# Kernel tuning notes

Hardware: AMD Instinct MI355X
Metric: run time of the kernel (lower is better)

Reference implementation:

```python
import jax, jax.numpy as jnp
import numpy as np

D_MODEL = 768
NUM_HEADS = 12
D_K = D_MODEL // NUM_HEADS


def setup_inputs() -> dict:
    key = jax.random.key(0)
    ks = jax.random.split(key, 9)
    B, S = 2, 4096
    x = jax.random.normal(ks[0], (B, S, D_MODEL), dtype=jnp.float32)
    s = 1.0 / np.sqrt(D_MODEL)
    Wq = jax.random.normal(ks[1], (D_MODEL, D_MODEL), dtype=jnp.float32) * s
    Wk = jax.random.normal(ks[2], (D_MODEL, D_MODEL), dtype=jnp.float32) * s
    Wv = jax.random.normal(ks[3], (D_MODEL, D_MODEL), dtype=jnp.float32) * s
    Wo = jax.random.normal(ks[4], (D_MODEL, D_MODEL), dtype=jnp.float32) * s
    bq = jnp.zeros((D_MODEL,), dtype=jnp.float32)
    bk = jnp.zeros((D_MODEL,), dtype=jnp.float32)
    bv = jnp.zeros((D_MODEL,), dtype=jnp.float32)
    bo = jnp.zeros((D_MODEL,), dtype=jnp.float32)
    return {"x": x, "Wq": Wq, "bq": bq, "Wk": Wk, "bk": bk,
            "Wv": Wv, "bv": bv, "Wo": Wo, "bo": bo}


def _split_heads(t):
    B, S, _ = t.shape
    return t.reshape(B, S, NUM_HEADS, D_K).transpose(0, 2, 1, 3)  # [B,H,S,d_k]


def reference(x, Wq, bq, Wk, bk, Wv, bv, Wo, bo):
    Q = _split_heads(x @ Wq.T + bq)
    K = _split_heads(x @ Wk.T + bk)
    V = _split_heads(x @ Wv.T + bv)
    scale = 1.0 / jnp.sqrt(jnp.float32(D_K))
    scores = jnp.einsum('bhqd,bhkd->bhqk', Q, K) * scale  # [B,H,S,S]
    attn = jax.nn.softmax(scores, axis=-1)
    out = jnp.einsum('bhqk,bhkd->bhqd', attn, V)          # [B,H,S,d_k]
    B, _, S, _ = out.shape
    out = out.transpose(0, 2, 1, 3).reshape(B, S, D_MODEL)
    return out @ Wo.T + bo
```

## Files before the change

kernel.cpp:

```cpp
#include <hip/hip_runtime.h>
#include <hip/hip_bf16.h>
#include <stdint.h>

typedef __hip_bfloat16 bf16;
typedef __attribute__((ext_vector_type(8))) short short8;
typedef __attribute__((ext_vector_type(4))) float f32x4;
typedef __attribute__((ext_vector_type(16))) float f32x16;

#define MFMA16(a, b, c) __builtin_amdgcn_mfma_f32_16x16x32_bf16((a), (b), (c), 0, 0, 0)
#define MFMA32(a, b, c) __builtin_amdgcn_mfma_f32_32x32x16_bf16((a), (b), (c), 0, 0, 0)

__device__ __forceinline__ unsigned short f2bf(float f) {
  bf16 h = __float2bfloat16(f);
  unsigned short u;
  __builtin_memcpy(&u, &h, 2);
  return u;
}

__device__ __forceinline__ uint32_t cvtpk(float lo, float hi) {
  uint32_t r;
  asm("v_cvt_pk_bf16_f32 %0, %1, %2" : "=v"(r) : "v"(lo), "v"(hi));
  return r;
}

__device__ __forceinline__ void pl32swap(uint32_t& a, uint32_t& b) {
  asm volatile("v_permlane32_swap_b32 %0, %1" : "+v"(a), "+v"(b));
}

__device__ __forceinline__ void gload_lds16(const void* g, void* l) {
  __builtin_amdgcn_global_load_lds(
      (const __attribute__((address_space(1))) uint32_t*)g,
      (__attribute__((address_space(3))) uint32_t*)l, 16, 0, 0);
}

__device__ __forceinline__ int swz_chunk(int row, int c) { return c ^ (row & 7); }

__global__ __launch_bounds__(256) void cvt_all(
    const float* __restrict__ x,
    const float* __restrict__ w0, const float* __restrict__ w1,
    const float* __restrict__ w2, const float* __restrict__ w3,
    bf16* __restrict__ xo,
    bf16* __restrict__ o0, bf16* __restrict__ o1,
    bf16* __restrict__ o2, bf16* __restrict__ o3) {
  int idx = blockIdx.x * 256 + threadIdx.x;
  const float* src;
  bf16* dst;
  int i;
  if (idx < 1572864) {
    src = x; dst = xo; i = idx;
  } else {
    int r = idx - 1572864;
    int w = r / 147456;
    i = r - w * 147456;
    src = (w == 0) ? w0 : (w == 1) ? w1 : (w == 2) ? w2 : w3;
    dst = (w == 0) ? o0 : (w == 1) ? o1 : (w == 2) ? o2 : o3;
  }
  float4 v = ((const float4*)src)[i];
  ushort4 u;
  u.x = f2bf(v.x); u.y = f2bf(v.y); u.z = f2bf(v.z); u.w = f2bf(v.w);
  ((ushort4*)dst)[i] = u;
}

__global__ __launch_bounds__(256, 4) void gemm_qkv(
    const bf16* __restrict__ A,
    const bf16* __restrict__ Wqb, const bf16* __restrict__ Wkb,
    const bf16* __restrict__ Wvb,
    const float* __restrict__ bq, const float* __restrict__ bk,
    const float* __restrict__ bv,
    bf16* __restrict__ Qh, bf16* __restrict__ Kh, bf16* __restrict__ Vh,
    float sq) {
  __shared__ bf16 As[128 * 64];
  __shared__ bf16 Bs[128 * 64];
  const int tid = threadIdx.x;
  const int lane = tid & 63, wid = tid >> 6;
  const int wr = wid >> 1, wc = wid & 1;
  const int l15 = lane & 15, lhi = lane >> 4;
  const int tm = blockIdx.x * 128;
  const int by = blockIdx.y;
  const int seg = by / 6;
  const int tn = (by - seg * 6) * 128;

  const bf16* B = (seg == 0) ? Wqb : (seg == 1) ? Wkb : Wvb;
  const float* bias = (seg == 0) ? bq : (seg == 1) ? bk : bv;
  bf16* dst = (seg == 0) ? Qh : (seg == 1) ? Kh : Vh;
  const float scale = (seg == 0) ? sq : 1.0f;
  const int K = 768;

  f32x4 zero = {0.f, 0.f, 0.f, 0.f};
  f32x4 acc[4][4];
  for (int i = 0; i < 4; ++i)
    for (int j = 0; j < 4; ++j) acc[i][j] = zero;

  for (int k0 = 0; k0 < K; k0 += 64) {
    __syncthreads();
    for (int it = 0; it < 4; ++it) {
      int o = (tid + it * 256) << 4;
      int row = o >> 7, c = (o >> 4) & 7;
      int sw = swz_chunk(row, c) << 4;
      gload_lds16((const char*)A + (((size_t)(tm + row) * K + k0) << 1) + sw, (char*)As + o);
      gload_lds16((const char*)B + (((size_t)(tn + row) * K + k0) << 1) + sw, (char*)Bs + o);
    }
    __syncthreads();
    for (int ks = 0; ks < 2; ++ks) {
      short8 af[4], bfr[4];
      for (int mi = 0; mi < 4; ++mi) {
        int row = wr * 64 + mi * 16 + l15;
        af[mi] = *(const short8*)((const char*)As + row * 128 +
                                  (swz_chunk(row, ks * 4 + lhi) << 4));
      }
      for (int ni = 0; ni < 4; ++ni) {
        int row = wc * 64 + ni * 16 + l15;
        bfr[ni] = *(const short8*)((const char*)Bs + row * 128 +
                                   (swz_chunk(row, ks * 4 + lhi) << 4));
      }
      for (int mi = 0; mi < 4; ++mi)
        for (int ni = 0; ni < 4; ++ni)
          acc[mi][ni] = MFMA16(af[mi], bfr[ni], acc[mi][ni]);
    }
  }

  for (int mi = 0; mi < 4; ++mi)
    for (int ni = 0; ni < 4; ++ni)
      for (int j = 0; j < 4; ++j) {
        int m = tm + wr * 64 + mi * 16 + lhi * 4 + j;
        int n = tn + wc * 64 + ni * 16 + l15;
        float v = (acc[mi][ni][j] + bias[n]) * scale;
        int b = m >> 12, s = m & 4095, h = n >> 6, d = n & 63;
        dst[(((size_t)(b * 12 + h) * 4096 + s) << 6) + d] = __float2bfloat16(v);
      }
}

__global__ __launch_bounds__(256, 4) void gemm_wo(
    const bf16* __restrict__ A, const bf16* __restrict__ B,
    const float* __restrict__ bias, float* __restrict__ C) {
  __shared__ bf16 As[128 * 64];
  __shared__ bf16 Bs[64 * 64];
  const int tid = threadIdx.x;
  const int lane = tid & 63, wid = tid >> 6;
  const int l15 = lane & 15, lhi = lane >> 4;
  const int tm = blockIdx.x * 128, tn = blockIdx.y * 64;
  const int K = 768;

  f32x4 zero = {0.f, 0.f, 0.f, 0.f};
  f32x4 acc[2][4];
  for (int i = 0; i < 2; ++i)
    for (int j = 0; j < 4; ++j) acc[i][j] = zero;

  for (int k0 = 0; k0 < K; k0 += 64) {
    __syncthreads();
    for (int it = 0; it < 4; ++it) {
      int o = (tid + it * 256) << 4;
      int row = o >> 7, c = (o >> 4) & 7;
      int sw = swz_chunk(row, c) << 4;
      gload_lds16((const char*)A + (((size_t)(tm + row) * K + k0) << 1) + sw, (char*)As + o);
    }
    for (int it = 0; it < 2; ++it) {
      int o = (tid + it * 256) << 4;
      int row = o >> 7, c = (o >> 4) & 7;
      int sw = swz_chunk(row, c) << 4;
      gload_lds16((const char*)B + (((size_t)(tn + row) * K + k0) << 1) + sw, (char*)Bs + o);
    }
    __syncthreads();
    for (int ks = 0; ks < 2; ++ks) {
      short8 af[2], bfr[4];
      for (int mi = 0; mi < 2; ++mi) {
        int row = wid * 32 + mi * 16 + l15;
        af[mi] = *(const short8*)((const char*)As + row * 128 +
                                  (swz_chunk(row, ks * 4 + lhi) << 4));
      }
      for (int ni = 0; ni < 4; ++ni) {
        int row = ni * 16 + l15;
        bfr[ni] = *(const short8*)((const char*)Bs + row * 128 +
                                   (swz_chunk(row, ks * 4 + lhi) << 4));
      }
      for (int mi = 0; mi < 2; ++mi)
        for (int ni = 0; ni < 4; ++ni)
          acc[mi][ni] = MFMA16(af[mi], bfr[ni], acc[mi][ni]);
    }
  }

  for (int mi = 0; mi < 2; ++mi)
    for (int ni = 0; ni < 4; ++ni)
      for (int j = 0; j < 4; ++j) {
        int m = tm + wid * 32 + mi * 16 + lhi * 4 + j;
        int n = tn + ni * 16 + l15;
        C[(size_t)m * 768 + n] = acc[mi][ni][j] + bias[n];
      }
}

__global__ __launch_bounds__(256) void transpose_v(const bf16* __restrict__ Vh,
                                                   bf16* __restrict__ VTh) {
  __shared__ bf16 T[64 * 64];
  const int tid = threadIdx.x;
  const int bh = blockIdx.x >> 6;
  const int t = blockIdx.x & 63;
  const char* src = (const char*)(Vh + ((size_t)bh * 4096 + t * 64) * 64);
  char* dst = (char*)(VTh + ((size_t)bh * 64) * 4096 + t * 64);

  const int rp = tid & 31, cc = tid >> 5;
  uint4 va = *(const uint4*)(src + (2 * rp) * 128 + cc * 16);
  uint4 vb = *(const uint4*)(src + (2 * rp + 1) * 128 + cc * 16);
  unsigned short a16[8], b16[8];
  __builtin_memcpy(a16, &va, 16);
  __builtin_memcpy(b16, &vb, 16);
#pragma unroll
  for (int jj = 0; jj < 8; ++jj) {
    uint32_t w = (uint32_t)a16[jj] | ((uint32_t)b16[jj] << 16);
    *(uint32_t*)((char*)T + (cc * 8 + jj) * 128 + (((rp >> 2) ^ jj) << 4) +
                 ((rp & 3) << 2)) = w;
  }
  __syncthreads();
  for (int it = 0; it < 2; ++it) {
    int idx = tid + it * 256;
    int d = idx >> 3, c = idx & 7;
    uint4 vv = *(const uint4*)((const char*)T + d * 128 + (swz_chunk(d, c) << 4));
    *(uint4*)(dst + (size_t)d * 8192 + c * 16) = vv;
  }
}

__global__ __launch_bounds__(256, 3) void attn_kernel(
    const bf16* __restrict__ Qh, const bf16* __restrict__ Kh,
    const bf16* __restrict__ VTh, bf16* __restrict__ AO) {
  __shared__ float4 smem4[34816 / 16];
  char* smraw = (char*)smem4;
#define KT(b) (smraw + (b) * 8192)
#define VT(b) (smraw + 16384 + (b) * 8192)
  float* OX = (float*)smraw;

  const int tid = threadIdx.x;
  const int lane = tid & 63, wid = tid >> 6;
  const int l31 = lane & 31, h = lane >> 5;
  const int qsub = wid & 1, kvh = wid >> 1;

  const int i = blockIdx.x;
  const int xcd = i & 7, slot = i >> 3;
  const int bh = xcd * 3 + (slot >> 5);
  const int qt = slot & 31;

  const size_t hb = (size_t)bh * 4096 * 64;
  const bf16* Qb = Qh + hb;
  const bf16* Kb = Kh + hb;
  const char* Vg0 = (const char*)(VTh + hb);
  const int qb = qt * 128 + qsub * 64;

  short8 qf[2][4];
#pragma unroll
  for (int j = 0; j < 2; ++j)
#pragma unroll
    for (int ki = 0; ki < 4; ++ki)
      qf[j][ki] = *(const short8*)((const char*)Qb + (size_t)(qb + 32 * j + l31) * 128 +
                                   ki * 32 + h * 16);

  f32x16 z16;
  for (int i2 = 0; i2 < 16; ++i2) z16[i2] = 0.f;
  f32x16 o00 = z16, o01 = z16, o10 = z16, o11 = z16;
  float psum0 = 0.f, psum1 = 0.f;

  const int krow = kvh * 32 + l31;

  for (int it = 0; it < 2; ++it) {
    int o = (tid + it * 256) << 4;
    int row = o >> 7, c = (o >> 4) & 7;
    int sw = swz_chunk(row, c) << 4;
    gload_lds16((const char*)Kb + row * 128 + sw, KT(0) + o);
    gload_lds16(Vg0 + row * 8192 + sw, VT(0) + o);
  }
  __syncthreads();

  int cur = 0;
  for (int kt = 0; kt < 64; ++kt) {
    if (kt < 63) {
      const char* Kg = (const char*)(Kb + (size_t)(kt + 1) * 4096);
      const char* Vg = Vg0 + (size_t)(kt + 1) * 128;
      char* Kd = KT(cur ^ 1);
      char* Vd = VT(cur ^ 1);
      for (int it = 0; it < 2; ++it) {
        int o = (tid + it * 256) << 4;
        int row = o >> 7, c = (o >> 4) & 7;
        int sw = swz_chunk(row, c) << 4;
        gload_lds16(Kg + row * 128 + sw, Kd + o);
        gload_lds16(Vg + row * 8192 + sw, Vd + o);
      }
    }

    const char* Kl = KT(cur);
    const char* Vl = VT(cur);

    f32x16 s0, s1;
    __builtin_amdgcn_s_setprio(1);
    {
      short8 kf = *(const short8*)(Kl + krow * 128 + (swz_chunk(krow, h) << 4));
      s0 = MFMA32(kf, qf[0][0], z16);
      s1 = MFMA32(kf, qf[1][0], z16);
    }
#pragma unroll
    for (int ki = 1; ki < 4; ++ki) {
      short8 kf = *(const short8*)(Kl + krow * 128 + (swz_chunk(krow, 2 * ki + h) << 4));
      s0 = MFMA32(kf, qf[0][ki], s0);
      s1 = MFMA32(kf, qf[1][ki], s1);
    }
    __builtin_amdgcn_s_setprio(0);

    short8 pb[2][2];
#pragma unroll
    for (int j = 0; j < 2; ++j) {
#pragma unroll
      for (int kk = 0; kk < 2; ++kk) {
        float p[8];
#pragma unroll
        for (int e = 0; e < 8; ++e)
          p[e] = __builtin_amdgcn_exp2f(j ? s1[8 * kk + e] : s0[8 * kk + e]);
        float ps = ((p[0] + p[1]) + (p[2] + p[3])) + ((p[4] + p[5]) + (p[6] + p[7]));
        if (j) psum1 += ps; else psum0 += ps;
        uint32_t A0 = cvtpk(p[0], p[1]), A1 = cvtpk(p[2], p[3]);
        uint32_t B0 = cvtpk(p[4], p[5]), B1 = cvtpk(p[6], p[7]);
        pl32swap(A0, B0);
        pl32swap(A1, B1);
        uint32_t w[4] = {A0, A1, B0, B1};
        short8 frag;
        __builtin_memcpy(&frag, w, 16);
        pb[j][kk] = frag;
      }
    }

    __builtin_amdgcn_s_setprio(1);
#pragma unroll
    for (int kk = 0; kk < 2; ++kk) {
      short8 v0 = *(const short8*)(Vl + l31 * 128 +
                                   (swz_chunk(l31, 4 * kvh + 2 * kk + h) << 4));
      short8 v1 = *(const short8*)(Vl + (32 + l31) * 128 +
                                   (swz_chunk(32 + l31, 4 * kvh + 2 * kk + h) << 4));
      o00 = MFMA32(v0, pb[0][kk], o00);
      o01 = MFMA32(v0, pb[1][kk], o01);
      o10 = MFMA32(v1, pb[0][kk], o10);
      o11 = MFMA32(v1, pb[1][kk], o11);
    }
    __builtin_amdgcn_s_setprio(0);

    __syncthreads();
    cur ^= 1;
  }

  psum0 += __shfl_xor(psum0, 32);
  psum1 += __shfl_xor(psum1, 32);

  float* W = OX + (size_t)(qsub * 64 + lane) * 68;
  if (kvh == 1) {
#pragma unroll
    for (int g = 0; g < 4; ++g) {
      *(float4*)(W + 0 * 16 + 4 * g) = make_float4(o00[4*g], o00[4*g+1], o00[4*g+2], o00[4*g+3]);
      *(float4*)(W + 1 * 16 + 4 * g) = make_float4(o01[4*g], o01[4*g+1], o01[4*g+2], o01[4*g+3]);
      *(float4*)(W + 2 * 16 + 4 * g) = make_float4(o10[4*g], o10[4*g+1], o10[4*g+2], o10[4*g+3]);
      *(float4*)(W + 3 * 16 + 4 * g) = make_float4(o11[4*g], o11[4*g+1], o11[4*g+2], o11[4*g+3]);
    }
    W[64] = psum0;
    W[65] = psum1;
  }
  __syncthreads();
  if (kvh == 0) {
#pragma unroll
    for (int g = 0; g < 4; ++g) {
      float4 a0 = *(const float4*)(W + 0 * 16 + 4 * g);
      float4 a1 = *(const float4*)(W + 1 * 16 + 4 * g);
      float4 a2 = *(const float4*)(W + 2 * 16 + 4 * g);
      float4 a3 = *(const float4*)(W + 3 * 16 + 4 * g);
      o00[4*g] += a0.x; o00[4*g+1] += a0.y; o00[4*g+2] += a0.z; o00[4*g+3] += a0.w;
      o01[4*g] += a1.x; o01[4*g+1] += a1.y; o01[4*g+2] += a1.z; o01[4*g+3] += a1.w;
      o10[4*g] += a2.x; o10[4*g+1] += a2.y; o10[4*g+2] += a2.z; o10[4*g+3] += a2.w;
      o11[4*g] += a3.x; o11[4*g+1] += a3.y; o11[4*g+2] += a3.z; o11[4*g+3] += a3.w;
    }
    psum0 += W[64];
    psum1 += W[65];
    float pinv0 = 1.0f / psum0;
    float pinv1 = 1.0f / psum1;

    const int b = bh / 12, hd = bh % 12;
#pragma unroll
    for (int j = 0; j < 2; ++j) {
      int q = qb + 32 * j + l31;
      char* base = (char*)AO + (((size_t)(b * 4096 + q)) * 768 + hd * 64) * 2;
      float pv = j ? pinv1 : pinv0;
#pragma unroll
      for (int t = 0; t < 2; ++t) {
#pragma unroll
        for (int u = 0; u < 4; ++u) {
          ushort4 us;
          float v0 = (t ? (j ? o11[4*u+0] : o10[4*u+0]) : (j ? o01[4*u+0] : o00[4*u+0]));
          float v1 = (t ? (j ? o11[4*u+1] : o10[4*u+1]) : (j ? o01[4*u+1] : o00[4*u+1]));
          float v2 = (t ? (j ? o11[4*u+2] : o10[4*u+2]) : (j ? o01[4*u+2] : o00[4*u+2]));
          float v3 = (t ? (j ? o11[4*u+3] : o10[4*u+3]) : (j ? o01[4*u+3] : o00[4*u+3]));
          us.x = f2bf(v0 * pv);
          us.y = f2bf(v1 * pv);
          us.z = f2bf(v2 * pv);
          us.w = f2bf(v3 * pv);
          int d0 = 32 * t + 8 * u + 4 * h;
          *(ushort4*)(base + d0 * 2) = us;
        }
      }
    }
  }
#undef KT
#undef VT
}

extern "C" void kernel_launch(void* const* d_in, const int* in_sizes, int n_in,
                              void* d_out, int out_size, void* d_ws, size_t ws_size,
                              hipStream_t stream) {
  (void)in_sizes; (void)n_in; (void)out_size; (void)ws_size;
  const float* x  = (const float*)d_in[0];
  const float* Wq = (const float*)d_in[1];
  const float* bq = (const float*)d_in[2];
  const float* Wk = (const float*)d_in[3];
  const float* bk = (const float*)d_in[4];
  const float* Wv = (const float*)d_in[5];
  const float* bv = (const float*)d_in[6];
  const float* Wo = (const float*)d_in[7];
  const float* bo = (const float*)d_in[8];

  char* ws = (char*)d_ws;
  bf16* Qh  = (bf16*)(ws + 0);
  bf16* Kh  = (bf16*)(ws + 12582912);
  bf16* Vh  = (bf16*)(ws + 25165824);
  bf16* xb  = (bf16*)(ws + 37748736);
  bf16* Wqb = (bf16*)(ws + 50331648);
  bf16* Wkb = (bf16*)(ws + 51511296);
  bf16* Wvb = (bf16*)(ws + 52690944);
  bf16* Wob = (bf16*)(ws + 53870592);
  bf16* VTh = xb;
  bf16* AO  = Vh;

  cvt_all<<<8448, 256, 0, stream>>>(x, Wq, Wk, Wv, Wo, xb, Wqb, Wkb, Wvb, Wob);

  const float SQ = 0.125f * 1.4426950408889634f;
  dim3 gq(64, 18);
  gemm_qkv<<<gq, 256, 0, stream>>>(xb, Wqb, Wkb, Wvb, bq, bk, bv,
                                   Qh, Kh, Vh, SQ);
  transpose_v<<<1536, 256, 0, stream>>>(Vh, VTh);
  attn_kernel<<<768, 256, 0, stream>>>(Qh, Kh, VTh, AO);
  dim3 gw(64, 12);
  gemm_wo<<<gw, 256, 0, stream>>>(AO, Wob, bo, (float*)d_out);
}
```

Before: 187.9 us.

## Write V pre-tiled from QKV GEMM and load K/V directly to registers in attention

The QKV GEMM epilogue now writes V in a tiled, transposed layout that matches the MFMA fragment order, which removes the separate transpose_v kernel launch and its extra pass over V. The attention kernel drops the LDS double-buffer and the per-iteration __syncthreads. It instead loads K and V fragments straight from global memory into registers, with two register sets ping-ponged to prefetch the next tile. Launch bounds drop from 3 to 2 blocks per SM to make room for the extra registers. The cost is reduced occupancy and loads that are no longer shared through LDS, so the two wave pairs of each block each read the same K/V tiles from global memory or cache.

```diff
diff --git a/kernel.cpp b/kernel.cpp
--- a/kernel.cpp
+++ b/kernel.cpp
@@ -67,7 +67,7 @@
     const bf16* __restrict__ Wvb,
     const float* __restrict__ bq, const float* __restrict__ bk,
     const float* __restrict__ bv,
-    bf16* __restrict__ Qh, bf16* __restrict__ Kh, bf16* __restrict__ Vh,
+    bf16* __restrict__ Qh, bf16* __restrict__ Kh, bf16* __restrict__ Vtt,
     float sq) {
   __shared__ bf16 As[128 * 64];
   __shared__ bf16 Bs[128 * 64];
@@ -82,7 +82,6 @@
 
   const bf16* B = (seg == 0) ? Wqb : (seg == 1) ? Wkb : Wvb;
   const float* bias = (seg == 0) ? bq : (seg == 1) ? bk : bv;
-  bf16* dst = (seg == 0) ? Qh : (seg == 1) ? Kh : Vh;
   const float scale = (seg == 0) ? sq : 1.0f;
   const int K = 768;
 
@@ -119,15 +118,34 @@
     }
   }
 
-  for (int mi = 0; mi < 4; ++mi)
-    for (int ni = 0; ni < 4; ++ni)
-      for (int j = 0; j < 4; ++j) {
-        int m = tm + wr * 64 + mi * 16 + lhi * 4 + j;
+  if (seg == 2) {
+    for (int mi = 0; mi < 4; ++mi)
+      for (int ni = 0; ni < 4; ++ni) {
+        int m0 = tm + wr * 64 + mi * 16 + lhi * 4;
         int n = tn + wc * 64 + ni * 16 + l15;
-        float v = (acc[mi][ni][j] + bias[n]) * scale;
-        int b = m >> 12, s = m & 4095, h = n >> 6, d = n & 63;
-        dst[(((size_t)(b * 12 + h) * 4096 + s) << 6) + d] = __float2bfloat16(v);
-      }
+        int b = m0 >> 12, s = m0 & 4095, hh = n >> 6, d = n & 63;
+        float bia = bias[n];
+        ushort4 us;
+        us.x = f2bf(acc[mi][ni][0] + bia);
+        us.y = f2bf(acc[mi][ni][1] + bia);
+        us.z = f2bf(acc[mi][ni][2] + bia);
+        us.w = f2bf(acc[mi][ni][3] + bia);
+        size_t e = (size_t)(b * 12 + hh) * 262144 + (size_t)(s >> 6) * 4096 +
+                   (size_t)((s >> 3) & 7) * 512 + d * 8 + (s & 7);
+        *(ushort4*)(Vtt + e) = us;
+      }
+  } else {
+    bf16* dst = (seg == 0) ? Qh : Kh;
+    for (int mi = 0; mi < 4; ++mi)
+      for (int ni = 0; ni < 4; ++ni)
+        for (int j = 0; j < 4; ++j) {
+          int m = tm + wr * 64 + mi * 16 + lhi * 4 + j;
+          int n = tn + wc * 64 + ni * 16 + l15;
+          float v = (acc[mi][ni][j] + bias[n]) * scale;
+          int b = m >> 12, s = m & 4095, hh = n >> 6, d = n & 63;
+          dst[(((size_t)(b * 12 + hh) * 4096 + s) << 6) + d] = __float2bfloat16(v);
+        }
+  }
 }
 
 __global__ __launch_bounds__(256, 4) void gemm_wo(
@@ -188,44 +206,11 @@
       }
 }
 
-__global__ __launch_bounds__(256) void transpose_v(const bf16* __restrict__ Vh,
-                                                   bf16* __restrict__ VTh) {
-  __shared__ bf16 T[64 * 64];
-  const int tid = threadIdx.x;
-  const int bh = blockIdx.x >> 6;
-  const int t = blockIdx.x & 63;
-  const char* src = (const char*)(Vh + ((size_t)bh * 4096 + t * 64) * 64);
-  char* dst = (char*)(VTh + ((size_t)bh * 64) * 4096 + t * 64);
-
-  const int rp = tid & 31, cc = tid >> 5;
-  uint4 va = *(const uint4*)(src + (2 * rp) * 128 + cc * 16);
-  uint4 vb = *(const uint4*)(src + (2 * rp + 1) * 128 + cc * 16);
-  unsigned short a16[8], b16[8];
-  __builtin_memcpy(a16, &va, 16);
-  __builtin_memcpy(b16, &vb, 16);
-#pragma unroll
-  for (int jj = 0; jj < 8; ++jj) {
-    uint32_t w = (uint32_t)a16[jj] | ((uint32_t)b16[jj] << 16);
-    *(uint32_t*)((char*)T + (cc * 8 + jj) * 128 + (((rp >> 2) ^ jj) << 4) +
-                 ((rp & 3) << 2)) = w;
-  }
-  __syncthreads();
-  for (int it = 0; it < 2; ++it) {
-    int idx = tid + it * 256;
-    int d = idx >> 3, c = idx & 7;
-    uint4 vv = *(const uint4*)((const char*)T + d * 128 + (swz_chunk(d, c) << 4));
-    *(uint4*)(dst + (size_t)d * 8192 + c * 16) = vv;
-  }
-}
-
-__global__ __launch_bounds__(256, 3) void attn_kernel(
+__global__ __launch_bounds__(256, 2) void attn_kernel(
     const bf16* __restrict__ Qh, const bf16* __restrict__ Kh,
-    const bf16* __restrict__ VTh, bf16* __restrict__ AO) {
+    const bf16* __restrict__ VTT, bf16* __restrict__ AO) {
   __shared__ float4 smem4[34816 / 16];
-  char* smraw = (char*)smem4;
-#define KT(b) (smraw + (b) * 8192)
-#define VT(b) (smraw + 16384 + (b) * 8192)
-  float* OX = (float*)smraw;
+  float* OX = (float*)smem4;
 
   const int tid = threadIdx.x;
   const int lane = tid & 63, wid = tid >> 6;
@@ -239,8 +224,8 @@
 
   const size_t hb = (size_t)bh * 4096 * 64;
   const bf16* Qb = Qh + hb;
-  const bf16* Kb = Kh + hb;
-  const char* Vg0 = (const char*)(VTh + hb);
+  const char* Kbc = (const char*)(Kh + hb);
+  const char* Vbc = (const char*)(VTT + hb);
   const int qb = qt * 128 + qsub * 64;
 
   short8 qf[2][4];
@@ -256,90 +241,82 @@
   f32x16 o00 = z16, o01 = z16, o10 = z16, o11 = z16;
   float psum0 = 0.f, psum1 = 0.f;
 
-  const int krow = kvh * 32 + l31;
-
-  for (int it = 0; it < 2; ++it) {
-    int o = (tid + it * 256) << 4;
-    int row = o >> 7, c = (o >> 4) & 7;
-    int sw = swz_chunk(row, c) << 4;
-    gload_lds16((const char*)Kb + row * 128 + sw, KT(0) + o);
-    gload_lds16(Vg0 + row * 8192 + sw, VT(0) + o);
-  }
-  __syncthreads();
-
-  int cur = 0;
-  for (int kt = 0; kt < 64; ++kt) {
-    if (kt < 63) {
-      const char* Kg = (const char*)(Kb + (size_t)(kt + 1) * 4096);
-      const char* Vg = Vg0 + (size_t)(kt + 1) * 128;
-      char* Kd = KT(cur ^ 1);
-      char* Vd = VT(cur ^ 1);
-      for (int it = 0; it < 2; ++it) {
-        int o = (tid + it * 256) << 4;
-        int row = o >> 7, c = (o >> 4) & 7;
-        int sw = swz_chunk(row, c) << 4;
-        gload_lds16(Kg + row * 128 + sw, Kd + o);
-        gload_lds16(Vg + row * 8192 + sw, Vd + o);
-      }
-    }
-
-    const char* Kl = KT(cur);
-    const char* Vl = VT(cur);
-
-    f32x16 s0, s1;
-    __builtin_amdgcn_s_setprio(1);
-    {
-      short8 kf = *(const short8*)(Kl + krow * 128 + (swz_chunk(krow, h) << 4));
-      s0 = MFMA32(kf, qf[0][0], z16);
-      s1 = MFMA32(kf, qf[1][0], z16);
-    }
-#pragma unroll
-    for (int ki = 1; ki < 4; ++ki) {
-      short8 kf = *(const short8*)(Kl + krow * 128 + (swz_chunk(krow, 2 * ki + h) << 4));
-      s0 = MFMA32(kf, qf[0][ki], s0);
-      s1 = MFMA32(kf, qf[1][ki], s1);
-    }
-    __builtin_amdgcn_s_setprio(0);
-
-    short8 pb[2][2];
-#pragma unroll
-    for (int j = 0; j < 2; ++j) {
-#pragma unroll
-      for (int kk = 0; kk < 2; ++kk) {
-        float p[8];
-#pragma unroll
-        for (int e = 0; e < 8; ++e)
-          p[e] = __builtin_amdgcn_exp2f(j ? s1[8 * kk + e] : s0[8 * kk + e]);
-        float ps = ((p[0] + p[1]) + (p[2] + p[3])) + ((p[4] + p[5]) + (p[6] + p[7]));
-        if (j) psum1 += ps; else psum0 += ps;
-        uint32_t A0 = cvtpk(p[0], p[1]), A1 = cvtpk(p[2], p[3]);
-        uint32_t B0 = cvtpk(p[4], p[5]), B1 = cvtpk(p[6], p[7]);
-        pl32swap(A0, B0);
-        pl32swap(A1, B1);
-        uint32_t w[4] = {A0, A1, B0, B1};
-        short8 frag;
-        __builtin_memcpy(&frag, w, 16);
-        pb[j][kk] = frag;
-      }
-    }
-
-    __builtin_amdgcn_s_setprio(1);
-#pragma unroll
-    for (int kk = 0; kk < 2; ++kk) {
-      short8 v0 = *(const short8*)(Vl + l31 * 128 +
-                                   (swz_chunk(l31, 4 * kvh + 2 * kk + h) << 4));
-      short8 v1 = *(const short8*)(Vl + (32 + l31) * 128 +
-                                   (swz_chunk(32 + l31, 4 * kvh + 2 * kk + h) << 4));
-      o00 = MFMA32(v0, pb[0][kk], o00);
-      o01 = MFMA32(v0, pb[1][kk], o01);
-      o10 = MFMA32(v1, pb[0][kk], o10);
-      o11 = MFMA32(v1, pb[1][kk], o11);
-    }
-    __builtin_amdgcn_s_setprio(0);
-
-    __syncthreads();
-    cur ^= 1;
-  }
+  const int koff = (kvh * 32 + l31) * 128 + h * 16;
+  const int voff = (4 * kvh + h) * 1024 + l31 * 16;
+
+#define ISSUE(kt, K0, K1, K2, K3, V00, V01, V10, V11)                    \
+  {                                                                      \
+    const char* kp = Kbc + (size_t)(kt) * 8192 + koff;                   \
+    K0 = *(const short8*)(kp);                                           \
+    K1 = *(const short8*)(kp + 32);                                      \
+    K2 = *(const short8*)(kp + 64);                                      \
+    K3 = *(const short8*)(kp + 96);                                      \
+    const char* vp = Vbc + (size_t)(kt) * 8192 + voff;                   \
+    V00 = *(const short8*)(vp);                                          \
+    V10 = *(const short8*)(vp + 512);                                    \
+    V01 = *(const short8*)(vp + 2048);                                   \
+    V11 = *(const short8*)(vp + 2048 + 512);                             \
+  }
+
+#define PHASE(K0, K1, K2, K3, V00, V01, V10, V11)                        \
+  {                                                                      \
+    f32x16 s0, s1;                                                       \
+    __builtin_amdgcn_s_setprio(1);                                       \
+    s0 = MFMA32(K0, qf[0][0], z16);                                      \
+    s1 = MFMA32(K0, qf[1][0], z16);                                      \
+    s0 = MFMA32(K1, qf[0][1], s0);                                       \
+    s1 = MFMA32(K1, qf[1][1], s1);                                       \
+    s0 = MFMA32(K2, qf[0][2], s0);                                       \
+    s1 = MFMA32(K2, qf[1][2], s1);                                       \
+    s0 = MFMA32(K3, qf[0][3], s0);                                       \
+    s1 = MFMA32(K3, qf[1][3], s1);                                       \
+    __builtin_amdgcn_s_setprio(0);                                       \
+    short8 pb[2][2];                                                     \
+    _Pragma("unroll")                                                    \
+    for (int j = 0; j < 2; ++j) {                                        \
+      _Pragma("unroll")                                                  \
+      for (int kk = 0; kk < 2; ++kk) {                                   \
+        float p[8];                                                      \
+        _Pragma("unroll")                                                \
+        for (int e = 0; e < 8; ++e)                                      \
+          p[e] = __builtin_amdgcn_exp2f(j ? s1[8 * kk + e] : s0[8 * kk + e]); \
+        float ps = ((p[0] + p[1]) + (p[2] + p[3])) + ((p[4] + p[5]) + (p[6] + p[7])); \
+        if (j) psum1 += ps; else psum0 += ps;                            \
+        uint32_t A0 = cvtpk(p[0], p[1]), A1 = cvtpk(p[2], p[3]);         \
+        uint32_t B0 = cvtpk(p[4], p[5]), B1 = cvtpk(p[6], p[7]);         \
+        pl32swap(A0, B0);                                                \
+        pl32swap(A1, B1);                                                \
+        uint32_t w_[4] = {A0, A1, B0, B1};                               \
+        short8 frag;                                                     \
+        __builtin_memcpy(&frag, w_, 16);                                 \
+        pb[j][kk] = frag;                                                \
+      }                                                                  \
+    }                                                                    \
+    __builtin_amdgcn_s_setprio(1);                                       \
+    o00 = MFMA32(V00, pb[0][0], o00);                                    \
+    o01 = MFMA32(V00, pb[1][0], o01);                                    \
+    o10 = MFMA32(V10, pb[0][0], o10);                                    \
+    o11 = MFMA32(V10, pb[1][0], o11);                                    \
+    o00 = MFMA32(V01, pb[0][1], o00);                                    \
+    o01 = MFMA32(V01, pb[1][1], o01);                                    \
+    o10 = MFMA32(V11, pb[0][1], o10);                                    \
+    o11 = MFMA32(V11, pb[1][1], o11);                                    \
+    __builtin_amdgcn_s_setprio(0);                                       \
+  }
+
+  short8 kA0, kA1, kA2, kA3, vA00, vA01, vA10, vA11;
+  short8 kB0, kB1, kB2, kB3, vB00, vB01, vB10, vB11;
+
+  ISSUE(0, kA0, kA1, kA2, kA3, vA00, vA01, vA10, vA11);
+  for (int kt = 0; kt < 64; kt += 2) {
+    ISSUE(kt + 1, kB0, kB1, kB2, kB3, vB00, vB01, vB10, vB11);
+    PHASE(kA0, kA1, kA2, kA3, vA00, vA01, vA10, vA11);
+    if (kt + 2 < 64)
+      ISSUE(kt + 2, kA0, kA1, kA2, kA3, vA00, vA01, vA10, vA11);
+    PHASE(kB0, kB1, kB2, kB3, vB00, vB01, vB10, vB11);
+  }
+#undef ISSUE
+#undef PHASE
 
   psum0 += __shfl_xor(psum0, 32);
   psum1 += __shfl_xor(psum1, 32);
@@ -399,8 +376,6 @@
       }
     }
   }
-#undef KT
-#undef VT
 }
 
 extern "C" void kernel_launch(void* const* d_in, const int* in_sizes, int n_in,
@@ -420,23 +395,21 @@
   char* ws = (char*)d_ws;
   bf16* Qh  = (bf16*)(ws + 0);
   bf16* Kh  = (bf16*)(ws + 12582912);
-  bf16* Vh  = (bf16*)(ws + 25165824);
+  bf16* VTT = (bf16*)(ws + 25165824);
   bf16* xb  = (bf16*)(ws + 37748736);
   bf16* Wqb = (bf16*)(ws + 50331648);
   bf16* Wkb = (bf16*)(ws + 51511296);
   bf16* Wvb = (bf16*)(ws + 52690944);
   bf16* Wob = (bf16*)(ws + 53870592);
-  bf16* VTh = xb;
-  bf16* AO  = Vh;
+  bf16* AO  = xb;
 
   cvt_all<<<8448, 256, 0, stream>>>(x, Wq, Wk, Wv, Wo, xb, Wqb, Wkb, Wvb, Wob);
 
   const float SQ = 0.125f * 1.4426950408889634f;
   dim3 gq(64, 18);
   gemm_qkv<<<gq, 256, 0, stream>>>(xb, Wqb, Wkb, Wvb, bq, bk, bv,
-                                   Qh, Kh, Vh, SQ);
-  transpose_v<<<1536, 256, 0, stream>>>(Vh, VTh);
-  attn_kernel<<<768, 256, 0, stream>>>(Qh, Kh, VTh, AO);
+                                   Qh, Kh, VTT, SQ);
+  attn_kernel<<<768, 256, 0, stream>>>(Qh, Kh, VTT, AO);
   dim3 gw(64, 12);
   gemm_wo<<<gw, 256, 0, stream>>>(AO, Wob, bo, (float*)d_out);
 }
```

Result: slower. 194.6 us (+3.5%).

## Fuse V transpose into QKV GEMM epilogue with a blocked chunked V layout

Applied to the files above, without the earlier changes.

The QKV GEMM epilogue for the V segment now writes a tiled, pre-transposed layout directly (64-key blocks, 8-key chunks per d), and the separate transpose_v kernel is removed. The attention kernel's V tile loads are adjusted to read from this layout into the same swizzled LDS arrangement. This removes one kernel launch and a full read plus write of V. In exchange, the V epilogue stores are 8-byte scattered writes rather than contiguous rows.

```diff
diff --git a/kernel.cpp b/kernel.cpp
--- a/kernel.cpp
+++ b/kernel.cpp
@@ -67,7 +67,7 @@
     const bf16* __restrict__ Wvb,
     const float* __restrict__ bq, const float* __restrict__ bk,
     const float* __restrict__ bv,
-    bf16* __restrict__ Qh, bf16* __restrict__ Kh, bf16* __restrict__ Vh,
+    bf16* __restrict__ Qh, bf16* __restrict__ Kh, bf16* __restrict__ Vtt,
     float sq) {
   __shared__ bf16 As[128 * 64];
   __shared__ bf16 Bs[128 * 64];
@@ -82,7 +82,6 @@
 
   const bf16* B = (seg == 0) ? Wqb : (seg == 1) ? Wkb : Wvb;
   const float* bias = (seg == 0) ? bq : (seg == 1) ? bk : bv;
-  bf16* dst = (seg == 0) ? Qh : (seg == 1) ? Kh : Vh;
   const float scale = (seg == 0) ? sq : 1.0f;
   const int K = 768;
 
@@ -119,15 +118,34 @@
     }
   }
 
-  for (int mi = 0; mi < 4; ++mi)
-    for (int ni = 0; ni < 4; ++ni)
-      for (int j = 0; j < 4; ++j) {
-        int m = tm + wr * 64 + mi * 16 + lhi * 4 + j;
+  if (seg == 2) {
+    for (int mi = 0; mi < 4; ++mi)
+      for (int ni = 0; ni < 4; ++ni) {
+        int m0 = tm + wr * 64 + mi * 16 + lhi * 4;
         int n = tn + wc * 64 + ni * 16 + l15;
-        float v = (acc[mi][ni][j] + bias[n]) * scale;
-        int b = m >> 12, s = m & 4095, h = n >> 6, d = n & 63;
-        dst[(((size_t)(b * 12 + h) * 4096 + s) << 6) + d] = __float2bfloat16(v);
-      }
+        int b = m0 >> 12, s = m0 & 4095, hh = n >> 6, d = n & 63;
+        float bia = bias[n];
+        ushort4 us;
+        us.x = f2bf(acc[mi][ni][0] + bia);
+        us.y = f2bf(acc[mi][ni][1] + bia);
+        us.z = f2bf(acc[mi][ni][2] + bia);
+        us.w = f2bf(acc[mi][ni][3] + bia);
+        size_t e = (size_t)(b * 12 + hh) * 262144 + (size_t)(s >> 6) * 4096 +
+                   (size_t)((s >> 3) & 7) * 512 + d * 8 + (s & 7);
+        *(ushort4*)(Vtt + e) = us;
+      }
+  } else {
+    bf16* dst = (seg == 0) ? Qh : Kh;
+    for (int mi = 0; mi < 4; ++mi)
+      for (int ni = 0; ni < 4; ++ni)
+        for (int j = 0; j < 4; ++j) {
+          int m = tm + wr * 64 + mi * 16 + lhi * 4 + j;
+          int n = tn + wc * 64 + ni * 16 + l15;
+          float v = (acc[mi][ni][j] + bias[n]) * scale;
+          int b = m >> 12, s = m & 4095, hh = n >> 6, d = n & 63;
+          dst[(((size_t)(b * 12 + hh) * 4096 + s) << 6) + d] = __float2bfloat16(v);
+        }
+  }
 }
 
 __global__ __launch_bounds__(256, 4) void gemm_wo(
@@ -188,39 +206,9 @@
       }
 }
 
-__global__ __launch_bounds__(256) void transpose_v(const bf16* __restrict__ Vh,
-                                                   bf16* __restrict__ VTh) {
-  __shared__ bf16 T[64 * 64];
-  const int tid = threadIdx.x;
-  const int bh = blockIdx.x >> 6;
-  const int t = blockIdx.x & 63;
-  const char* src = (const char*)(Vh + ((size_t)bh * 4096 + t * 64) * 64);
-  char* dst = (char*)(VTh + ((size_t)bh * 64) * 4096 + t * 64);
-
-  const int rp = tid & 31, cc = tid >> 5;
-  uint4 va = *(const uint4*)(src + (2 * rp) * 128 + cc * 16);
-  uint4 vb = *(const uint4*)(src + (2 * rp + 1) * 128 + cc * 16);
-  unsigned short a16[8], b16[8];
-  __builtin_memcpy(a16, &va, 16);
-  __builtin_memcpy(b16, &vb, 16);
-#pragma unroll
-  for (int jj = 0; jj < 8; ++jj) {
-    uint32_t w = (uint32_t)a16[jj] | ((uint32_t)b16[jj] << 16);
-    *(uint32_t*)((char*)T + (cc * 8 + jj) * 128 + (((rp >> 2) ^ jj) << 4) +
-                 ((rp & 3) << 2)) = w;
-  }
-  __syncthreads();
-  for (int it = 0; it < 2; ++it) {
-    int idx = tid + it * 256;
-    int d = idx >> 3, c = idx & 7;
-    uint4 vv = *(const uint4*)((const char*)T + d * 128 + (swz_chunk(d, c) << 4));
-    *(uint4*)(dst + (size_t)d * 8192 + c * 16) = vv;
-  }
-}
-
 __global__ __launch_bounds__(256, 3) void attn_kernel(
     const bf16* __restrict__ Qh, const bf16* __restrict__ Kh,
-    const bf16* __restrict__ VTh, bf16* __restrict__ AO) {
+    const bf16* __restrict__ VTT, bf16* __restrict__ AO) {
   __shared__ float4 smem4[34816 / 16];
   char* smraw = (char*)smem4;
 #define KT(b) (smraw + (b) * 8192)
@@ -237,10 +225,10 @@
   const int bh = xcd * 3 + (slot >> 5);
   const int qt = slot & 31;
 
-  const size_t hb = (size_t)bh * 4096 * 64;
+  const size_t hb = (size_t)bh * 262144;
   const bf16* Qb = Qh + hb;
   const bf16* Kb = Kh + hb;
-  const char* Vg0 = (const char*)(VTh + hb);
+  const char* Vbc = (const char*)(VTT + hb);
   const int qb = qt * 128 + qsub * 64;
 
   short8 qf[2][4];
@@ -261,9 +249,8 @@
   for (int it = 0; it < 2; ++it) {
     int o = (tid + it * 256) << 4;
     int row = o >> 7, c = (o >> 4) & 7;
-    int sw = swz_chunk(row, c) << 4;
-    gload_lds16((const char*)Kb + row * 128 + sw, KT(0) + o);
-    gload_lds16(Vg0 + row * 8192 + sw, VT(0) + o);
+    gload_lds16((const char*)Kb + row * 128 + (swz_chunk(row, c) << 4), KT(0) + o);
+    gload_lds16(Vbc + (swz_chunk(row, c) << 10) + (row << 4), VT(0) + o);
   }
   __syncthreads();
 
@@ -271,15 +258,14 @@
   for (int kt = 0; kt < 64; ++kt) {
     if (kt < 63) {
       const char* Kg = (const char*)(Kb + (size_t)(kt + 1) * 4096);
-      const char* Vg = Vg0 + (size_t)(kt + 1) * 128;
+      const char* Vg = Vbc + (size_t)(kt + 1) * 8192;
       char* Kd = KT(cur ^ 1);
       char* Vd = VT(cur ^ 1);
       for (int it = 0; it < 2; ++it) {
         int o = (tid + it * 256) << 4;
         int row = o >> 7, c = (o >> 4) & 7;
-        int sw = swz_chunk(row, c) << 4;
-        gload_lds16(Kg + row * 128 + sw, Kd + o);
-        gload_lds16(Vg + row * 8192 + sw, Vd + o);
+        gload_lds16(Kg + row * 128 + (swz_chunk(row, c) << 4), Kd + o);
+        gload_lds16(Vg + (swz_chunk(row, c) << 10) + (row << 4), Vd + o);
       }
     }
 
@@ -420,23 +406,21 @@
   char* ws = (char*)d_ws;
   bf16* Qh  = (bf16*)(ws + 0);
   bf16* Kh  = (bf16*)(ws + 12582912);
-  bf16* Vh  = (bf16*)(ws + 25165824);
+  bf16* VTT = (bf16*)(ws + 25165824);
   bf16* xb  = (bf16*)(ws + 37748736);
   bf16* Wqb = (bf16*)(ws + 50331648);
   bf16* Wkb = (bf16*)(ws + 51511296);
   bf16* Wvb = (bf16*)(ws + 52690944);
   bf16* Wob = (bf16*)(ws + 53870592);
-  bf16* VTh = xb;
-  bf16* AO  = Vh;
+  bf16* AO  = xb;
 
   cvt_all<<<8448, 256, 0, stream>>>(x, Wq, Wk, Wv, Wo, xb, Wqb, Wkb, Wvb, Wob);
 
   const float SQ = 0.125f * 1.4426950408889634f;
   dim3 gq(64, 18);
   gemm_qkv<<<gq, 256, 0, stream>>>(xb, Wqb, Wkb, Wvb, bq, bk, bv,
-                                   Qh, Kh, Vh, SQ);
-  transpose_v<<<1536, 256, 0, stream>>>(Vh, VTh);
-  attn_kernel<<<768, 256, 0, stream>>>(Qh, Kh, VTh, AO);
+                                   Qh, Kh, VTT, SQ);
+  attn_kernel<<<768, 256, 0, stream>>>(Qh, Kh, VTT, AO);
   dim3 gw(64, 12);
   gemm_wo<<<gw, 256, 0, stream>>>(AO, Wob, bo, (float*)d_out);
 }
```

After: 180.3 us, median of 2. -4.0%, faster.
